# Kernel tuning notes

Measured on AMD Instinct MI355X. Metric: run time of the kernel, lower is better.

The kernel has to match this reference:

```python
import jax, jax.numpy as jnp
import numpy as np

B, LQ, S, D, H = 8, 1024, 256, 1024, 16
HD = D // H
LN_EPS = 1e-5


def layer_norm(x, g, b):
    m = jnp.mean(x, axis=-1, keepdims=True)
    v = jnp.mean((x - m) ** 2, axis=-1, keepdims=True)
    return (x - m) / jnp.sqrt(v + LN_EPS) * g + b


def setup_inputs() -> dict:
    key = jax.random.key(0)
    ks = jax.random.split(key, 12)
    sc = 0.02
    p = lambda k, shp: jax.random.normal(k, shp, dtype=jnp.float32) * sc
    return {
        "memory": jax.random.normal(ks[0], (B, LQ, D // 2), dtype=jnp.float32),
        "gaze_features": jax.random.normal(ks[1], (B, LQ, D // 2), dtype=jnp.float32),
        "text_features": jax.random.normal(ks[2], (B, S, D), dtype=jnp.float32),
        "w_in": p(ks[3], (3 * D, D)),  # packed q,k,v in_proj (torch MHA layout)
        "b_in": jnp.zeros((3 * D,), jnp.float32),
        "w_o": p(ks[4], (D, D)),
        "b_o": jnp.zeros((D,), jnp.float32),
        "w1": p(ks[5], (D, D)),
        "b1": jnp.zeros((D,), jnp.float32),
        "w2": p(ks[6], (D, D)),
        "b2": jnp.zeros((D,), jnp.float32),
        "g1": jnp.ones((D,), jnp.float32),
        "be1": jnp.zeros((D,), jnp.float32),
        "g2": jnp.ones((D,), jnp.float32),
        "be2": jnp.zeros((D,), jnp.float32),
    }


def reference(memory, gaze_features, text_features, w_in, b_in, w_o, b_o,
              w1, b1, w2, b2, g1, be1, g2, be2):
    combined = jnp.concatenate([memory, gaze_features], axis=-1)  # [B, LQ, D]
    wq, wk, wv = w_in[:D], w_in[D:2 * D], w_in[2 * D:]
    bq, bk, bv = b_in[:D], b_in[D:2 * D], b_in[2 * D:]

    q = (combined @ wq.T + bq).reshape(B, LQ, H, HD)
    k = (text_features @ wk.T + bk).reshape(B, S, H, HD)
    v = (text_features @ wv.T + bv).reshape(B, S, H, HD)

    scores = jnp.einsum("bqhd,bkhd->bhqk", q, k) / jnp.sqrt(jnp.float32(HD))
    attn_w = jax.nn.softmax(scores, axis=-1)
    ctx = jnp.einsum("bhqk,bkhd->bqhd", attn_w, v).reshape(B, LQ, D)
    attn_output = ctx @ w_o.T + b_o  # [B, LQ, D]

    # dual FFN branches share linear1/linear2 (as in the source); dropout = eval identity
    ffn = jax.nn.relu(attn_output @ w1.T + b1) @ w2.T + b2
    refpoint_embed = layer_norm(ffn, g1, be1)
    tgt = layer_norm(ffn, g2, be2)

    # vectorized box decode (replaces the per-element Python loop)
    s = jax.nn.sigmoid(attn_output[..., :4])
    xc, yc, w, h = s[..., 0], s[..., 1], s[..., 2], s[..., 3]
    init_box_proposal = jnp.stack(
        [xc - w / 2, yc - h / 2, xc + w / 2, yc + h / 2], axis=-1)  # [B, LQ, 4]

    return refpoint_embed, tgt, init_box_proposal
```

## Files before the change

### kernel.cpp

```cpp
#include <hip/hip_runtime.h>


typedef unsigned short u16;
typedef unsigned int u32;
typedef __bf16 bf16x8 __attribute__((ext_vector_type(8)));
typedef float f32x4 __attribute__((ext_vector_type(4)));
typedef u16 u16x4 __attribute__((ext_vector_type(4)));

__device__ __forceinline__ u16 f2bf(float f) {
  u32 u = __builtin_bit_cast(u32, f);
  u += 0x7fffu + ((u >> 16) & 1u);
  return (u16)(u >> 16);
}
__device__ __forceinline__ float bf2f(u16 h) {
  u32 u = ((u32)h) << 16;
  return __builtin_bit_cast(float, u);
}

__global__ void probe_kernel(const u32* __restrict__ g1w, u32* __restrict__ flag) {
  *flag = (g1w[0] == 0x3F800000u) ? 1u : 0u;
}

__global__ __launch_bounds__(256) void cvt_kernel(
    const u32* __restrict__ flag, u16* __restrict__ dst,
    const void* s0, const void* s1, const void* s2, const void* s3,
    const void* s4, const void* s5, const void* s6, const void* s7,
    const void* s8, const void* s9, const void* s10, const void* s11,
    const void* s12, const void* s13, const void* s14)
{
  const u32 cum[16] = {0u, 4194304u, 8388608u, 10485760u, 13631488u, 13634560u,
                       14683136u, 14684160u, 15732736u, 15733760u, 16782336u,
                       16783360u, 16784384u, 16785408u, 16786432u, 16787456u};
  const void* srcs[15] = {s0, s1, s2, s3, s4, s5, s6, s7, s8, s9, s10, s11, s12, s13, s14};
  u32 base = (blockIdx.x * 256u + threadIdx.x) * 8u;
  if (base >= 16787456u) return;
  int idx = 0;
#pragma unroll
  for (int i = 1; i < 15; ++i) if (base >= cum[i]) idx = i;
  u32 off = base - cum[idx];
  if (*flag) {
    const float* s = (const float*)srcs[idx] + off;
    float4 a = ((const float4*)s)[0];
    float4 b = ((const float4*)s)[1];
    u16 t[8] = {f2bf(a.x), f2bf(a.y), f2bf(a.z), f2bf(a.w),
                f2bf(b.x), f2bf(b.y), f2bf(b.z), f2bf(b.w)};
    *(uint4*)(dst + base) = *(const uint4*)t;
  } else {
    *(uint4*)(dst + base) = *(const uint4*)((const u16*)srcs[idx] + off);
  }
}

__device__ __forceinline__ void gemm_core(
    u16* sA, u16* sB,
    const u16* A0, const u16* A1, int Ksplit, int lda0, int lda1,
    const u16* W, const u16* bias, void* out, int N, int K,
    int mode, int lg, int m0, int n0)
{
  const int tid = threadIdx.x;
  const int wave = tid >> 6, lane = tid & 63;
  const int quad = lane >> 4, l16 = lane & 15;
  const int wm = wave >> 1, wn = wave & 1;

  f32x4 acc[4][4];
#pragma unroll
  for (int i = 0; i < 4; ++i)
#pragma unroll
    for (int j = 0; j < 4; ++j) acc[i][j] = (f32x4){0.f, 0.f, 0.f, 0.f};

  for (int k0 = 0; k0 < K; k0 += 128) {
#pragma unroll
    for (int qi = 0; qi < 8; ++qi) {
      int p = (wave * 8 + qi) * 64 + lane;
      int row = p >> 4;
      int c = (p & 15) ^ (row & 7);
      int gk = k0 + (c << 3);
      const u16* srcA = (gk < Ksplit) ? (A0 + (size_t)(m0 + row) * lda0 + gk)
                                      : (A1 + (size_t)(m0 + row) * lda1 + (gk - Ksplit));
      __builtin_amdgcn_global_load_lds(
          (const __attribute__((address_space(1))) void*)srcA,
          (__attribute__((address_space(3))) void*)&sA[(size_t)(wave * 8 + qi) * 512],
          16, 0, 0);
      const u16* srcB = W + (size_t)(n0 + row) * K + gk;
      __builtin_amdgcn_global_load_lds(
          (const __attribute__((address_space(1))) void*)srcB,
          (__attribute__((address_space(3))) void*)&sB[(size_t)(wave * 8 + qi) * 512],
          16, 0, 0);
    }
    __syncthreads();
#pragma unroll
    for (int ks = 0; ks < 4; ++ks) {
      const int ch = (ks << 2) + quad;
      bf16x8 af[4], bw[4];
#pragma unroll
      for (int i = 0; i < 4; ++i) {
        int row = wm * 64 + i * 16 + l16;
        af[i] = *(const bf16x8*)&sA[(row << 7) + ((ch ^ (row & 7)) << 3)];
      }
#pragma unroll
      for (int j = 0; j < 4; ++j) {
        int row = wn * 64 + j * 16 + l16;
        bw[j] = *(const bf16x8*)&sB[(row << 7) + ((ch ^ (row & 7)) << 3)];
      }
#pragma unroll
      for (int i = 0; i < 4; ++i)
#pragma unroll
        for (int j = 0; j < 4; ++j)
          acc[i][j] = __builtin_amdgcn_mfma_f32_16x16x32_bf16(af[i], bw[j], acc[i][j], 0, 0, 0);
    }
    __syncthreads();
  }

#pragma unroll
  for (int i = 0; i < 4; ++i) {
#pragma unroll
    for (int j = 0; j < 4; ++j) {
      int n = n0 + wn * 64 + j * 16 + l16;
      float bv = bf2f(bias[n - n0 + n0]);
#pragma unroll
      for (int rr = 0; rr < 4; ++rr) {
        int m = m0 + wm * 64 + i * 16 + quad * 4 + rr;
        float val = acc[i][j][rr] + bv;
        if (mode == 1) val = fmaxf(val, 0.f);
        if (mode == 2) {
          ((float*)out)[(size_t)m * N + n] = val;
        } else if (mode <= 1) {
          ((u16*)out)[(size_t)m * N + n] = f2bf(val);
        } else if (mode == 3) {
          int b = m >> lg, l = m & ((1 << lg) - 1);
          int h = n >> 6, d = n & 63;
          ((u16*)out)[((size_t)((b * 16 + h)) << (lg + 6)) + (l << 6) + d] = f2bf(val);
        } else {
          int b = m >> lg, s = m & ((1 << lg) - 1);
          int h = n >> 6, d = n & 63;
          ((u16*)out)[((size_t)(((b * 16 + h) << 6) + d) << lg) + s] = f2bf(val);
        }
      }
    }
  }
}

__global__ __launch_bounds__(256) void gemm_bt(
    const u16* __restrict__ A0, const u16* __restrict__ W,
    const u16* __restrict__ bias, void* __restrict__ out,
    int N, int K, int mode, int lg)
{
  __shared__ u16 sA[128 * 128];
  __shared__ u16 sB[128 * 128];
  const int m0 = blockIdx.y * 128, n0 = blockIdx.x * 128;
  gemm_core(sA, sB, A0, A0, K, K, K, W, bias, out, N, K, mode, lg, m0, n0);
}

__global__ __launch_bounds__(256) void qkv_gemm(
    const u16* __restrict__ mem, const u16* __restrict__ gaze,
    const u16* __restrict__ text, const u16* __restrict__ w_in,
    const u16* __restrict__ b_in,
    u16* __restrict__ q, u16* __restrict__ k, u16* __restrict__ v)
{
  __shared__ u16 sA[128 * 128];
  __shared__ u16 sB[128 * 128];
  int bid = blockIdx.x;
  if (bid < 512) {
    int m0 = (bid >> 3) * 128, n0 = (bid & 7) * 128;
    gemm_core(sA, sB, mem, gaze, 512, 512, 512, w_in, b_in, q,
              1024, 1024, 3, 10, m0, n0);
  } else if (bid < 640) {
    int t = bid - 512;
    int m0 = (t >> 3) * 128, n0 = (t & 7) * 128;
    gemm_core(sA, sB, text, text, 1024, 1024, 1024, w_in + 1048576, b_in + 1024, k,
              1024, 1024, 3, 8, m0, n0);
  } else {
    int t = bid - 640;
    int m0 = (t >> 3) * 128, n0 = (t & 7) * 128;
    gemm_core(sA, sB, text, text, 1024, 1024, 1024, w_in + 2097152, b_in + 2048, v,
              1024, 1024, 4, 8, m0, n0);
  }
}

__global__ __launch_bounds__(256) void attn_kernel(
    const u16* __restrict__ q, const u16* __restrict__ k,
    const u16* __restrict__ v, u16* __restrict__ ctx)
{
  __shared__ u16 sV[64 * 256];
  __shared__ u16 sKP[256 * 64];
  const int tid = threadIdx.x;
  const int wave = tid >> 6, lane = tid & 63;
  const int quad = lane >> 4, l16 = lane & 15;
  const int qb = blockIdx.x, bh = blockIdx.y;

  {
    int rr = tid >> 3, c8 = (tid & 7) << 3;
    const u16* kb = k + (size_t)bh * 256 * 64;
#pragma unroll
    for (int p = 0; p < 8; ++p) {
      int row = p * 32 + rr;
      uint4 val = *(const uint4*)(kb + row * 64 + c8);
      *(uint4*)&sKP[(row << 6) + ((((c8 >> 3) ^ (row & 7))) << 3)] = val;
    }
    int r2 = tid >> 5, c8b = (tid & 31) << 3;
    const u16* vb = v + (size_t)bh * 64 * 256;
#pragma unroll
    for (int p = 0; p < 8; ++p) {
      int row = p * 8 + r2;
      uint4 val = *(const uint4*)(vb + (row << 8) + c8b);
      *(uint4*)&sV[(row << 8) + ((((c8b >> 3) ^ (row & 7))) << 3)] = val;
    }
  }
  bf16x8 aq[2];
  {
    const u16* qrow = q + ((size_t)bh * 1024 + qb * 64 + wave * 16 + l16) * 64 + quad * 8;
    aq[0] = *(const bf16x8*)(qrow);
    aq[1] = *(const bf16x8*)(qrow + 32);
  }
  __syncthreads();

  f32x4 sc[16];
#pragma unroll
  for (int nt = 0; nt < 16; ++nt) sc[nt] = (f32x4){0.f, 0.f, 0.f, 0.f};
#pragma unroll
  for (int ks = 0; ks < 2; ++ks) {
    const int ch = (ks << 2) + quad;
#pragma unroll
    for (int nt = 0; nt < 16; ++nt) {
      int row = nt * 16 + l16;
      bf16x8 bk = *(const bf16x8*)&sKP[(row << 6) + ((ch ^ (row & 7)) << 3)];
      sc[nt] = __builtin_amdgcn_mfma_f32_16x16x32_bf16(aq[ks], bk, sc[nt], 0, 0, 0);
    }
  }
#pragma unroll
  for (int rr = 0; rr < 4; ++rr) {
    float mx = -1e30f;
#pragma unroll
    for (int nt = 0; nt < 16; ++nt) mx = fmaxf(mx, sc[nt][rr]);
    for (int off = 1; off < 16; off <<= 1) mx = fmaxf(mx, __shfl_xor(mx, off, 64));
    float sum = 0.f;
#pragma unroll
    for (int nt = 0; nt < 16; ++nt) {
      float p = __expf((sc[nt][rr] - mx) * 0.125f);
      sc[nt][rr] = p; sum += p;
    }
    for (int off = 1; off < 16; off <<= 1) sum += __shfl_xor(sum, off, 64);
    float inv = 1.f / sum;
#pragma unroll
    for (int nt = 0; nt < 16; ++nt) sc[nt][rr] *= inv;
  }
  __syncthreads();
#pragma unroll
  for (int nt = 0; nt < 16; ++nt)
#pragma unroll
    for (int rr = 0; rr < 4; ++rr) {
      int row = wave * 16 + quad * 4 + rr;
      int col = nt * 16 + l16;
      sKP[(row << 8) + (((col >> 3) ^ (row & 7)) << 3) + (col & 7)] = f2bf(sc[nt][rr]);
    }
  __syncthreads();

  f32x4 o[4];
#pragma unroll
  for (int j = 0; j < 4; ++j) o[j] = (f32x4){0.f, 0.f, 0.f, 0.f};
#pragma unroll
  for (int ks = 0; ks < 8; ++ks) {
    const int ch = (ks << 2) + quad;
    int prow = wave * 16 + l16;
    bf16x8 ap = *(const bf16x8*)&sKP[(prow << 8) + ((ch ^ (prow & 7)) << 3)];
#pragma unroll
    for (int j = 0; j < 4; ++j) {
      int vrow = j * 16 + l16;
      bf16x8 bv = *(const bf16x8*)&sV[(vrow << 8) + ((ch ^ (vrow & 7)) << 3)];
      o[j] = __builtin_amdgcn_mfma_f32_16x16x32_bf16(ap, bv, o[j], 0, 0, 0);
    }
  }
  const int b = bh >> 4, h = bh & 15;
#pragma unroll
  for (int j = 0; j < 4; ++j)
#pragma unroll
    for (int rr = 0; rr < 4; ++rr) {
      int m = qb * 64 + wave * 16 + quad * 4 + rr;
      int d = h * 64 + j * 16 + l16;
      ctx[((size_t)b * 1024 + m) * 1024 + d] = f2bf(o[j][rr]);
    }
}

__global__ __launch_bounds__(256) void ln_kernel(
    const u32* __restrict__ flag, const float* __restrict__ ffn,
    const u16* __restrict__ g1, const u16* __restrict__ be1,
    const u16* __restrict__ g2, const u16* __restrict__ be2,
    void* __restrict__ outv)
{
  const int row = blockIdx.x, tid = threadIdx.x;
  const float4 x4 = ((const float4*)(ffn + (size_t)row * 1024))[tid];
  float s = x4.x + x4.y + x4.z + x4.w;
  float s2 = x4.x * x4.x + x4.y * x4.y + x4.z * x4.z + x4.w * x4.w;
  for (int m = 32; m >= 1; m >>= 1) { s += __shfl_xor(s, m, 64); s2 += __shfl_xor(s2, m, 64); }
  __shared__ float red[8];
  int wave = tid >> 6;
  if ((tid & 63) == 0) { red[wave] = s; red[4 + wave] = s2; }
  __syncthreads();
  s = red[0] + red[1] + red[2] + red[3];
  s2 = red[4] + red[5] + red[6] + red[7];
  float mean = s * (1.f / 1024.f);
  float var = s2 * (1.f / 1024.f) - mean * mean;
  float inv = rsqrtf(var + 1e-5f);
  int c = tid * 4;
  float y[4] = {(x4.x - mean) * inv, (x4.y - mean) * inv, (x4.z - mean) * inv, (x4.w - mean) * inv};
  float v1[4], v2[4];
#pragma unroll
  for (int i = 0; i < 4; ++i) {
    v1[i] = y[i] * bf2f(g1[c + i]) + bf2f(be1[c + i]);
    v2[i] = y[i] * bf2f(g2[c + i]) + bf2f(be2[c + i]);
  }
  if (*flag) {
    float* fo = (float*)outv;
    *(float4*)(fo + (size_t)row * 1024 + c) = make_float4(v1[0], v1[1], v1[2], v1[3]);
    *(float4*)(fo + 8388608 + (size_t)row * 1024 + c) = make_float4(v2[0], v2[1], v2[2], v2[3]);
  } else {
    u16* out = (u16*)outv;
    u16x4 o1, o2;
#pragma unroll
    for (int i = 0; i < 4; ++i) { o1[i] = f2bf(v1[i]); o2[i] = f2bf(v2[i]); }
    *(u16x4*)(out + (size_t)row * 1024 + c) = o1;
    *(u16x4*)(out + 8388608 + (size_t)row * 1024 + c) = o2;
  }
}

__global__ __launch_bounds__(256) void box_kernel(
    const u32* __restrict__ flag, const u16* __restrict__ attn, void* __restrict__ outv)
{
  int m = blockIdx.x * 256 + threadIdx.x;
  u16x4 a = *(const u16x4*)(attn + (size_t)m * 1024);
  float sv[4];
#pragma unroll
  for (int i = 0; i < 4; ++i) sv[i] = 1.f / (1.f + __expf(-bf2f(a[i])));
  float o0 = sv[0] - sv[2] * 0.5f, o1 = sv[1] - sv[3] * 0.5f;
  float o2 = sv[0] + sv[2] * 0.5f, o3 = sv[1] + sv[3] * 0.5f;
  if (*flag) {
    float* fo = (float*)outv + 16777216;
    *(float4*)(fo + (size_t)m * 4) = make_float4(o0, o1, o2, o3);
  } else {
    u16* bo = (u16*)outv + 16777216;
    u16x4 o; o[0] = f2bf(o0); o[1] = f2bf(o1); o[2] = f2bf(o2); o[3] = f2bf(o3);
    *(u16x4*)(bo + (size_t)m * 4) = o;
  }
}

extern "C" void kernel_launch(void* const* d_in, const int* in_sizes, int n_in,
                              void* d_out, int out_size, void* d_ws, size_t ws_size,
                              hipStream_t stream) {
  u16* C = (u16*)d_ws;
  u16* c_mem  = C;
  u16* c_gaze = C + 4194304;
  u16* c_text = C + 8388608;
  u16* c_win  = C + 10485760;
  u16* c_bin  = C + 13631488;
  u16* c_wo   = C + 13634560;
  u16* c_bo   = C + 14683136;
  u16* c_w1   = C + 14684160;
  u16* c_b1   = C + 15732736;
  u16* c_w2   = C + 15733760;
  u16* c_b2   = C + 16782336;
  u16* c_g1   = C + 16783360;
  u16* c_be1  = C + 16784384;
  u16* c_g2   = C + 16785408;
  u16* c_be2  = C + 16786432;
  u32* flag   = (u32*)(C + 16787456);
  u16* B2     = C + 16787488;
  u16* q        = B2;
  u16* k        = B2 + 8388608;
  u16* v        = B2 + 10485760;
  u16* ctx      = B2 + 12582912;
  u16* attn_out = B2 + 20971520;
  u16* h1       = B2 + 29360128;
  float* ffn    = (float*)B2;

  dim3 blk(256);
  probe_kernel<<<1, 1, 0, stream>>>((const u32*)d_in[11], flag);
  cvt_kernel<<<dim3(8197), blk, 0, stream>>>(flag, C,
      d_in[0], d_in[1], d_in[2], d_in[3], d_in[4], d_in[5], d_in[6], d_in[7],
      d_in[8], d_in[9], d_in[10], d_in[11], d_in[12], d_in[13], d_in[14]);

  qkv_gemm<<<dim3(768), blk, 0, stream>>>(c_mem, c_gaze, c_text, c_win, c_bin, q, k, v);
  attn_kernel<<<dim3(16, 128), blk, 0, stream>>>(q, k, v, ctx);
  gemm_bt<<<dim3(8, 64), blk, 0, stream>>>(ctx, c_wo, c_bo, attn_out, 1024, 1024, 0, 0);
  gemm_bt<<<dim3(8, 64), blk, 0, stream>>>(attn_out, c_w1, c_b1, h1, 1024, 1024, 1, 0);
  gemm_bt<<<dim3(8, 64), blk, 0, stream>>>(h1, c_w2, c_b2, ffn, 1024, 1024, 2, 0);
  ln_kernel<<<dim3(8192), blk, 0, stream>>>(flag, ffn, c_g1, c_be1, c_g2, c_be2, d_out);
  box_kernel<<<dim3(32), blk, 0, stream>>>(flag, attn_out, d_out);
}
```

Before: 320.5 us.

## Fuse all stages into one persistent cooperative kernel with grid syncs

Replaces the nine separate launches (probe, convert, QKV GEMM, attention, three GEMMs, layernorm, box) with one cooperative persistent kernel of 512 blocks that loops over tiles and separates stages with grid.sync. The aim is to remove per-launch overhead and inter-kernel gaps. In exchange the QKV stage runs 768 tiles over 512 blocks, which is imbalanced, occupancy is capped by the launch bounds, and grid syncs add their own cost. A fallback to separate launches runs if the cooperative launch fails.

```diff
diff --git a/kernel.cpp b/kernel.cpp
--- a/kernel.cpp
+++ b/kernel.cpp
@@ -1,4 +1,7 @@
 #include <hip/hip_runtime.h>
+#include <hip/hip_cooperative_groups.h>
+
+namespace cg = cooperative_groups;
 
 
 typedef unsigned short u16;
@@ -7,6 +10,12 @@
 typedef float f32x4 __attribute__((ext_vector_type(4)));
 typedef u16 u16x4 __attribute__((ext_vector_type(4)));
 
+struct MArgs {
+  const void* in[15];
+  void* out;
+  u16* ws;
+};
+
 __device__ __forceinline__ u16 f2bf(float f) {
   u32 u = __builtin_bit_cast(u32, f);
   u += 0x7fffu + ((u >> 16) & 1u);
@@ -17,28 +26,37 @@
   return __builtin_bit_cast(float, u);
 }
 
-__global__ void probe_kernel(const u32* __restrict__ g1w, u32* __restrict__ flag) {
-  *flag = (g1w[0] == 0x3F800000u) ? 1u : 0u;
-}
-
-__global__ __launch_bounds__(256) void cvt_kernel(
-    const u32* __restrict__ flag, u16* __restrict__ dst,
-    const void* s0, const void* s1, const void* s2, const void* s3,
-    const void* s4, const void* s5, const void* s6, const void* s7,
-    const void* s8, const void* s9, const void* s10, const void* s11,
-    const void* s12, const void* s13, const void* s14)
-{
+struct WsPtrs {
+  u16 *c_mem, *c_gaze, *c_text, *c_win, *c_bin, *c_wo, *c_bo, *c_w1, *c_b1,
+      *c_w2, *c_b2, *c_g1, *c_be1, *c_g2, *c_be2;
+  u16 *q, *k, *v, *ctx, *attn_out, *h1;
+  float* ffn;
+};
+__device__ __forceinline__ WsPtrs wsp(u16* C) {
+  WsPtrs w;
+  w.c_mem = C;                 w.c_gaze = C + 4194304;   w.c_text = C + 8388608;
+  w.c_win = C + 10485760;      w.c_bin = C + 13631488;   w.c_wo = C + 13634560;
+  w.c_bo = C + 14683136;       w.c_w1 = C + 14684160;    w.c_b1 = C + 15732736;
+  w.c_w2 = C + 15733760;       w.c_b2 = C + 16782336;    w.c_g1 = C + 16783360;
+  w.c_be1 = C + 16784384;      w.c_g2 = C + 16785408;    w.c_be2 = C + 16786432;
+  u16* B2 = C + 16787488;
+  w.q = B2;                    w.k = B2 + 8388608;       w.v = B2 + 10485760;
+  w.ctx = B2 + 12582912;       w.attn_out = B2 + 20971520; w.h1 = B2 + 29360128;
+  w.ffn = (float*)B2;
+  return w;
+}
+
+__device__ __forceinline__ void cvt_chunk(bool f32in, u16* dst,
+                                          const void* const* srcs, u32 c8) {
   const u32 cum[16] = {0u, 4194304u, 8388608u, 10485760u, 13631488u, 13634560u,
                        14683136u, 14684160u, 15732736u, 15733760u, 16782336u,
                        16783360u, 16784384u, 16785408u, 16786432u, 16787456u};
-  const void* srcs[15] = {s0, s1, s2, s3, s4, s5, s6, s7, s8, s9, s10, s11, s12, s13, s14};
-  u32 base = (blockIdx.x * 256u + threadIdx.x) * 8u;
-  if (base >= 16787456u) return;
+  u32 base = c8 * 8u;
   int idx = 0;
 #pragma unroll
   for (int i = 1; i < 15; ++i) if (base >= cum[i]) idx = i;
   u32 off = base - cum[idx];
-  if (*flag) {
+  if (f32in) {
     const float* s = (const float*)srcs[idx] + off;
     float4 a = ((const float4*)s)[0];
     float4 b = ((const float4*)s)[1];
@@ -115,7 +133,7 @@
 #pragma unroll
     for (int j = 0; j < 4; ++j) {
       int n = n0 + wn * 64 + j * 16 + l16;
-      float bv = bf2f(bias[n - n0 + n0]);
+      float bv = bf2f(bias[n]);
 #pragma unroll
       for (int rr = 0; rr < 4; ++rr) {
         int m = m0 + wm * 64 + i * 16 + quad * 4 + rr;
@@ -139,57 +157,17 @@
   }
 }
 
-__global__ __launch_bounds__(256) void gemm_bt(
-    const u16* __restrict__ A0, const u16* __restrict__ W,
-    const u16* __restrict__ bias, void* __restrict__ out,
-    int N, int K, int mode, int lg)
+__device__ __forceinline__ void attn_tile(
+    u16* sV, u16* sKP,
+    const u16* qg, const u16* kg, const u16* vg, u16* ctx, int qb, int bh)
 {
-  __shared__ u16 sA[128 * 128];
-  __shared__ u16 sB[128 * 128];
-  const int m0 = blockIdx.y * 128, n0 = blockIdx.x * 128;
-  gemm_core(sA, sB, A0, A0, K, K, K, W, bias, out, N, K, mode, lg, m0, n0);
-}
-
-__global__ __launch_bounds__(256) void qkv_gemm(
-    const u16* __restrict__ mem, const u16* __restrict__ gaze,
-    const u16* __restrict__ text, const u16* __restrict__ w_in,
-    const u16* __restrict__ b_in,
-    u16* __restrict__ q, u16* __restrict__ k, u16* __restrict__ v)
-{
-  __shared__ u16 sA[128 * 128];
-  __shared__ u16 sB[128 * 128];
-  int bid = blockIdx.x;
-  if (bid < 512) {
-    int m0 = (bid >> 3) * 128, n0 = (bid & 7) * 128;
-    gemm_core(sA, sB, mem, gaze, 512, 512, 512, w_in, b_in, q,
-              1024, 1024, 3, 10, m0, n0);
-  } else if (bid < 640) {
-    int t = bid - 512;
-    int m0 = (t >> 3) * 128, n0 = (t & 7) * 128;
-    gemm_core(sA, sB, text, text, 1024, 1024, 1024, w_in + 1048576, b_in + 1024, k,
-              1024, 1024, 3, 8, m0, n0);
-  } else {
-    int t = bid - 640;
-    int m0 = (t >> 3) * 128, n0 = (t & 7) * 128;
-    gemm_core(sA, sB, text, text, 1024, 1024, 1024, w_in + 2097152, b_in + 2048, v,
-              1024, 1024, 4, 8, m0, n0);
-  }
-}
-
-__global__ __launch_bounds__(256) void attn_kernel(
-    const u16* __restrict__ q, const u16* __restrict__ k,
-    const u16* __restrict__ v, u16* __restrict__ ctx)
-{
-  __shared__ u16 sV[64 * 256];
-  __shared__ u16 sKP[256 * 64];
   const int tid = threadIdx.x;
   const int wave = tid >> 6, lane = tid & 63;
   const int quad = lane >> 4, l16 = lane & 15;
-  const int qb = blockIdx.x, bh = blockIdx.y;
 
   {
     int rr = tid >> 3, c8 = (tid & 7) << 3;
-    const u16* kb = k + (size_t)bh * 256 * 64;
+    const u16* kb = kg + (size_t)bh * 16384;
 #pragma unroll
     for (int p = 0; p < 8; ++p) {
       int row = p * 32 + rr;
@@ -197,7 +175,7 @@
       *(uint4*)&sKP[(row << 6) + ((((c8 >> 3) ^ (row & 7))) << 3)] = val;
     }
     int r2 = tid >> 5, c8b = (tid & 31) << 3;
-    const u16* vb = v + (size_t)bh * 64 * 256;
+    const u16* vb = vg + (size_t)bh * 16384;
 #pragma unroll
     for (int p = 0; p < 8; ++p) {
       int row = p * 8 + r2;
@@ -207,7 +185,7 @@
   }
   bf16x8 aq[2];
   {
-    const u16* qrow = q + ((size_t)bh * 1024 + qb * 64 + wave * 16 + l16) * 64 + quad * 8;
+    const u16* qrow = qg + ((size_t)bh * 1024 + qb * 64 + wave * 16 + l16) * 64 + quad * 8;
     aq[0] = *(const bf16x8*)(qrow);
     aq[1] = *(const bf16x8*)(qrow + 32);
   }
@@ -280,23 +258,21 @@
     }
 }
 
-__global__ __launch_bounds__(256) void ln_kernel(
-    const u32* __restrict__ flag, const float* __restrict__ ffn,
-    const u16* __restrict__ g1, const u16* __restrict__ be1,
-    const u16* __restrict__ g2, const u16* __restrict__ be2,
-    void* __restrict__ outv)
+__device__ __forceinline__ void ln_row(
+    float* redf, const float* ffn,
+    const u16* g1, const u16* be1, const u16* g2, const u16* be2,
+    void* outv, bool f32out, int row)
 {
-  const int row = blockIdx.x, tid = threadIdx.x;
+  const int tid = threadIdx.x;
   const float4 x4 = ((const float4*)(ffn + (size_t)row * 1024))[tid];
   float s = x4.x + x4.y + x4.z + x4.w;
   float s2 = x4.x * x4.x + x4.y * x4.y + x4.z * x4.z + x4.w * x4.w;
   for (int m = 32; m >= 1; m >>= 1) { s += __shfl_xor(s, m, 64); s2 += __shfl_xor(s2, m, 64); }
-  __shared__ float red[8];
-  int wave = tid >> 6;
-  if ((tid & 63) == 0) { red[wave] = s; red[4 + wave] = s2; }
+  int wv = tid >> 6;
+  if ((tid & 63) == 0) { redf[wv] = s; redf[4 + wv] = s2; }
   __syncthreads();
-  s = red[0] + red[1] + red[2] + red[3];
-  s2 = red[4] + red[5] + red[6] + red[7];
+  s = redf[0] + redf[1] + redf[2] + redf[3];
+  s2 = redf[4] + redf[5] + redf[6] + redf[7];
   float mean = s * (1.f / 1024.f);
   float var = s2 * (1.f / 1024.f) - mean * mean;
   float inv = rsqrtf(var + 1e-5f);
@@ -308,7 +284,7 @@
     v1[i] = y[i] * bf2f(g1[c + i]) + bf2f(be1[c + i]);
     v2[i] = y[i] * bf2f(g2[c + i]) + bf2f(be2[c + i]);
   }
-  if (*flag) {
+  if (f32out) {
     float* fo = (float*)outv;
     *(float4*)(fo + (size_t)row * 1024 + c) = make_float4(v1[0], v1[1], v1[2], v1[3]);
     *(float4*)(fo + 8388608 + (size_t)row * 1024 + c) = make_float4(v2[0], v2[1], v2[2], v2[3]);
@@ -322,17 +298,14 @@
   }
 }
 
-__global__ __launch_bounds__(256) void box_kernel(
-    const u32* __restrict__ flag, const u16* __restrict__ attn, void* __restrict__ outv)
-{
-  int m = blockIdx.x * 256 + threadIdx.x;
+__device__ __forceinline__ void box_one(const u16* attn, void* outv, bool f32out, int m) {
   u16x4 a = *(const u16x4*)(attn + (size_t)m * 1024);
   float sv[4];
 #pragma unroll
   for (int i = 0; i < 4; ++i) sv[i] = 1.f / (1.f + __expf(-bf2f(a[i])));
   float o0 = sv[0] - sv[2] * 0.5f, o1 = sv[1] - sv[3] * 0.5f;
   float o2 = sv[0] + sv[2] * 0.5f, o3 = sv[1] + sv[3] * 0.5f;
-  if (*flag) {
+  if (f32out) {
     float* fo = (float*)outv + 16777216;
     *(float4*)(fo + (size_t)m * 4) = make_float4(o0, o1, o2, o3);
   } else {
@@ -342,46 +315,136 @@
   }
 }
 
+__global__ __launch_bounds__(256, 2) void mega_kernel(MArgs a) {
+  __shared__ u16 lds[32768];
+  cg::grid_group grid = cg::this_grid();
+  const int bid = blockIdx.x;
+  const u32 gtid = bid * 256u + threadIdx.x;
+  WsPtrs w = wsp(a.ws);
+  const bool f32io = (((const u32*)a.in[11])[0] == 0x3F800000u);
+
+  for (u32 c8 = gtid; c8 < 2098432u; c8 += 131072u)
+    cvt_chunk(f32io, a.ws, a.in, c8);
+  grid.sync();
+
+  for (int t = bid; t < 768; t += 512) {
+    if (t < 512) {
+      gemm_core(lds, lds + 16384, w.c_mem, w.c_gaze, 512, 512, 512,
+                w.c_win, w.c_bin, w.q, 1024, 1024, 3, 10, (t >> 3) * 128, (t & 7) * 128);
+    } else if (t < 640) {
+      int u = t - 512;
+      gemm_core(lds, lds + 16384, w.c_text, w.c_text, 1024, 1024, 1024,
+                w.c_win + 1048576, w.c_bin + 1024, w.k, 1024, 1024, 3, 8,
+                (u >> 3) * 128, (u & 7) * 128);
+    } else {
+      int u = t - 640;
+      gemm_core(lds, lds + 16384, w.c_text, w.c_text, 1024, 1024, 1024,
+                w.c_win + 2097152, w.c_bin + 2048, w.v, 1024, 1024, 4, 8,
+                (u >> 3) * 128, (u & 7) * 128);
+    }
+  }
+  grid.sync();
+
+  for (int t = bid; t < 2048; t += 512) {
+    __syncthreads();
+    attn_tile(lds, lds + 16384, w.q, w.k, w.v, w.ctx, t & 15, t >> 4);
+  }
+  grid.sync();
+
+  gemm_core(lds, lds + 16384, w.ctx, w.ctx, 1024, 1024, 1024,
+            w.c_wo, w.c_bo, w.attn_out, 1024, 1024, 0, 0,
+            (bid >> 3) * 128, (bid & 7) * 128);
+  grid.sync();
+
+  gemm_core(lds, lds + 16384, w.attn_out, w.attn_out, 1024, 1024, 1024,
+            w.c_w1, w.c_b1, w.h1, 1024, 1024, 1, 0,
+            (bid >> 3) * 128, (bid & 7) * 128);
+  grid.sync();
+
+  gemm_core(lds, lds + 16384, w.h1, w.h1, 1024, 1024, 1024,
+            w.c_w2, w.c_b2, w.ffn, 1024, 1024, 2, 0,
+            (bid >> 3) * 128, (bid & 7) * 128);
+  grid.sync();
+
+  if (gtid < 8192u) box_one(w.attn_out, a.out, f32io, (int)gtid);
+  for (int row = bid; row < 8192; row += 512) {
+    ln_row((float*)lds, w.ffn, w.c_g1, w.c_be1, w.c_g2, w.c_be2, a.out, f32io, row);
+    __syncthreads();
+  }
+}
+
+__global__ __launch_bounds__(256) void cvt_fb(MArgs a) {
+  u32 c8 = blockIdx.x * 256u + threadIdx.x;
+  if (c8 >= 2098432u) return;
+  const bool f32io = (((const u32*)a.in[11])[0] == 0x3F800000u);
+  cvt_chunk(f32io, a.ws, a.in, c8);
+}
+__global__ __launch_bounds__(256) void qkv_fb(MArgs a) {
+  __shared__ u16 lds[32768];
+  WsPtrs w = wsp(a.ws);
+  int t = blockIdx.x;
+  if (t < 512) {
+    gemm_core(lds, lds + 16384, w.c_mem, w.c_gaze, 512, 512, 512,
+              w.c_win, w.c_bin, w.q, 1024, 1024, 3, 10, (t >> 3) * 128, (t & 7) * 128);
+  } else if (t < 640) {
+    int u = t - 512;
+    gemm_core(lds, lds + 16384, w.c_text, w.c_text, 1024, 1024, 1024,
+              w.c_win + 1048576, w.c_bin + 1024, w.k, 1024, 1024, 3, 8,
+              (u >> 3) * 128, (u & 7) * 128);
+  } else {
+    int u = t - 640;
+    gemm_core(lds, lds + 16384, w.c_text, w.c_text, 1024, 1024, 1024,
+              w.c_win + 2097152, w.c_bin + 2048, w.v, 1024, 1024, 4, 8,
+              (u >> 3) * 128, (u & 7) * 128);
+  }
+}
+__global__ __launch_bounds__(256) void attn_fb(MArgs a) {
+  __shared__ u16 lds[32768];
+  WsPtrs w = wsp(a.ws);
+  attn_tile(lds, lds + 16384, w.q, w.k, w.v, w.ctx, blockIdx.x, blockIdx.y);
+}
+__global__ __launch_bounds__(256) void gemm_fb(MArgs a, int which) {
+  __shared__ u16 lds[32768];
+  WsPtrs w = wsp(a.ws);
+  int m0 = (blockIdx.x >> 3) * 128, n0 = (blockIdx.x & 7) * 128;
+  if (which == 0)
+    gemm_core(lds, lds + 16384, w.ctx, w.ctx, 1024, 1024, 1024,
+              w.c_wo, w.c_bo, w.attn_out, 1024, 1024, 0, 0, m0, n0);
+  else if (which == 1)
+    gemm_core(lds, lds + 16384, w.attn_out, w.attn_out, 1024, 1024, 1024,
+              w.c_w1, w.c_b1, w.h1, 1024, 1024, 1, 0, m0, n0);
+  else
+    gemm_core(lds, lds + 16384, w.h1, w.h1, 1024, 1024, 1024,
+              w.c_w2, w.c_b2, w.ffn, 1024, 1024, 2, 0, m0, n0);
+}
+__global__ __launch_bounds__(256) void lnbox_fb(MArgs a) {
+  __shared__ float redf[8];
+  WsPtrs w = wsp(a.ws);
+  const bool f32io = (((const u32*)a.in[11])[0] == 0x3F800000u);
+  u32 gtid = blockIdx.x * 256u + threadIdx.x;
+  if (gtid < 8192u) box_one(w.attn_out, a.out, f32io, (int)gtid);
+  ln_row(redf, w.ffn, w.c_g1, w.c_be1, w.c_g2, w.c_be2, a.out, f32io, blockIdx.x);
+}
+
 extern "C" void kernel_launch(void* const* d_in, const int* in_sizes, int n_in,
                               void* d_out, int out_size, void* d_ws, size_t ws_size,
                               hipStream_t stream) {
-  u16* C = (u16*)d_ws;
-  u16* c_mem  = C;
-  u16* c_gaze = C + 4194304;
-  u16* c_text = C + 8388608;
-  u16* c_win  = C + 10485760;
-  u16* c_bin  = C + 13631488;
-  u16* c_wo   = C + 13634560;
-  u16* c_bo   = C + 14683136;
-  u16* c_w1   = C + 14684160;
-  u16* c_b1   = C + 15732736;
-  u16* c_w2   = C + 15733760;
-  u16* c_b2   = C + 16782336;
-  u16* c_g1   = C + 16783360;
-  u16* c_be1  = C + 16784384;
-  u16* c_g2   = C + 16785408;
-  u16* c_be2  = C + 16786432;
-  u32* flag   = (u32*)(C + 16787456);
-  u16* B2     = C + 16787488;
-  u16* q        = B2;
-  u16* k        = B2 + 8388608;
-  u16* v        = B2 + 10485760;
-  u16* ctx      = B2 + 12582912;
-  u16* attn_out = B2 + 20971520;
-  u16* h1       = B2 + 29360128;
-  float* ffn    = (float*)B2;
-
-  dim3 blk(256);
-  probe_kernel<<<1, 1, 0, stream>>>((const u32*)d_in[11], flag);
-  cvt_kernel<<<dim3(8197), blk, 0, stream>>>(flag, C,
-      d_in[0], d_in[1], d_in[2], d_in[3], d_in[4], d_in[5], d_in[6], d_in[7],
-      d_in[8], d_in[9], d_in[10], d_in[11], d_in[12], d_in[13], d_in[14]);
-
-  qkv_gemm<<<dim3(768), blk, 0, stream>>>(c_mem, c_gaze, c_text, c_win, c_bin, q, k, v);
-  attn_kernel<<<dim3(16, 128), blk, 0, stream>>>(q, k, v, ctx);
-  gemm_bt<<<dim3(8, 64), blk, 0, stream>>>(ctx, c_wo, c_bo, attn_out, 1024, 1024, 0, 0);
-  gemm_bt<<<dim3(8, 64), blk, 0, stream>>>(attn_out, c_w1, c_b1, h1, 1024, 1024, 1, 0);
-  gemm_bt<<<dim3(8, 64), blk, 0, stream>>>(h1, c_w2, c_b2, ffn, 1024, 1024, 2, 0);
-  ln_kernel<<<dim3(8192), blk, 0, stream>>>(flag, ffn, c_g1, c_be1, c_g2, c_be2, d_out);
-  box_kernel<<<dim3(32), blk, 0, stream>>>(flag, attn_out, d_out);
-}
+  MArgs ma;
+  for (int i = 0; i < 15; ++i) ma.in[i] = d_in[i];
+  ma.out = d_out;
+  ma.ws = (u16*)d_ws;
+
+  void* params[] = { &ma };
+  hipError_t err = hipLaunchCooperativeKernel(mega_kernel, dim3(512), dim3(256),
+                                              params, 0u, stream);
+  if (err != hipSuccess) {
+    dim3 blk(256);
+    cvt_fb<<<dim3(8197), blk, 0, stream>>>(ma);
+    qkv_fb<<<dim3(768), blk, 0, stream>>>(ma);
+    attn_fb<<<dim3(16, 128), blk, 0, stream>>>(ma);
+    gemm_fb<<<dim3(512), blk, 0, stream>>>(ma, 0);
+    gemm_fb<<<dim3(512), blk, 0, stream>>>(ma, 1);
+    gemm_fb<<<dim3(512), blk, 0, stream>>>(ma, 2);
+    lnbox_fb<<<dim3(8192), blk, 0, stream>>>(ma);
+  }
+}
```

After: 713.9 us. 123% more time.
